# Performance work log

Hardware: AMD Instinct MI355X
Metric: run time of the kernel (lower is better)

Reference implementation:

```python
import jax, jax.numpy as jnp
import numpy as np
import math

B, T, C, NH = 4, 2048, 1024, 16
D = C // NH  # 64, rotary_dim == D

def _rope_tables():
    inv_freq = 1.0 / (10000.0 ** (np.arange(0, D, 2, dtype=np.float32) / D))
    t = np.arange(T, dtype=np.float32)
    freqs = np.outer(t, inv_freq)                 # [T, D/2]
    emb = np.concatenate([freqs, freqs], axis=-1)  # [T, D]
    return jnp.asarray(np.cos(emb))[None], jnp.asarray(np.sin(emb))[None]  # [1,T,D]

def setup_inputs() -> dict:
    key = jax.random.key(0)
    ks = jax.random.split(key, 3)
    x = jax.random.normal(ks[0], (B, T, C), dtype=jnp.float32)
    w_attn = jax.random.normal(ks[1], (3 * C, C), dtype=jnp.float32) * (1.0 / math.sqrt(C))
    b_attn = jnp.zeros((3 * C,), dtype=jnp.float32)
    w_proj = jax.random.normal(ks[2], (C, C), dtype=jnp.float32) * (1.0 / math.sqrt(C))
    b_proj = jnp.zeros((C,), dtype=jnp.float32)
    cos, sin = _rope_tables()
    return {"x": x, "w_attn": w_attn, "b_attn": b_attn,
            "w_proj": w_proj, "b_proj": b_proj, "cos": cos, "sin": sin}

def _rotate_half(u):
    u1, u2 = jnp.split(u, 2, axis=-1)
    return jnp.concatenate([-u2, u1], axis=-1)

def reference(x, w_attn, b_attn, w_proj, b_proj, cos, sin):
    Bx, Tx, Cx = x.shape
    nh, d = NH, Cx // NH
    # fused QKV projection (torch Linear: y = x @ W^T + b)
    qkv = x @ w_attn.T + b_attn                      # [B,T,3C]
    q, k, v = jnp.split(qkv, 3, axis=-1)
    q = q.reshape(Bx, Tx, nh, d).transpose(0, 2, 1, 3)  # [B,nh,T,d]
    k = k.reshape(Bx, Tx, nh, d).transpose(0, 2, 1, 3)
    v = v.reshape(Bx, Tx, nh, d).transpose(0, 2, 1, 3)
    # RoPE (rotary_dim == d, full head)
    c = cos[:, None, :, :]  # [1,1,T,d]
    s = sin[:, None, :, :]
    q = q * c + _rotate_half(q) * s
    k = k * c + _rotate_half(k) * s
    # naive causal attention
    scores = jnp.einsum("bhqd,bhkd->bhqk", q, k) / math.sqrt(d)
    causal = jnp.tril(jnp.ones((Tx, Tx), dtype=bool))
    scores = jnp.where(causal[None, None], scores, -jnp.inf)
    att = jax.nn.softmax(scores, axis=-1)
    y = jnp.einsum("bhqk,bhkd->bhqd", att, v)        # [B,nh,T,d]
    y = y.transpose(0, 2, 1, 3).reshape(Bx, Tx, Cx)
    return y @ w_proj.T + b_proj
```

## Files before the change

kernel.cpp:

```cpp
#include <hip/hip_runtime.h>

typedef __bf16 bf16_t;
typedef bf16_t bf16x8 __attribute__((ext_vector_type(8)));
typedef bf16_t bf16x4 __attribute__((ext_vector_type(4)));
typedef float f32x4 __attribute__((ext_vector_type(4)));

constexpr int BATCH = 4, SEQ = 2048, CH = 1024, NHEAD = 16, HD = 64;
constexpr int BM = 128, BN = 128, BKK = 32;

#define LGKM_FENCE() __asm__ __volatile__("s_waitcnt lgkmcnt(0)" ::: "memory")
#define VM_FENCE() __asm__ __volatile__("s_waitcnt vmcnt(0)" ::: "memory")
#define REORDER_FENCE() __asm__ __volatile__("" ::: "memory")

__device__ __forceinline__ void g2lds16(const bf16_t* g, bf16_t* l) {
  __builtin_amdgcn_global_load_lds((__attribute__((address_space(1))) void*)(g),
                                   (__attribute__((address_space(3))) void*)(l),
                                   16, 0, 0);
}

__device__ __forceinline__ f32x4 mfma16(bf16x8 a, bf16x8 b, f32x4 c) {
  return __builtin_amdgcn_mfma_f32_16x16x32_bf16(a, b, c, 0, 0, 0);
}

__global__ __launch_bounds__(256) void cvt_kernel(const float4* __restrict__ src,
                                                  ushort4* __restrict__ dst, int n4) {
  int i = blockIdx.x * 256 + threadIdx.x;
  if (i >= n4) return;
  float4 f = src[i];
  ushort4 o;
  o.x = __builtin_bit_cast(unsigned short, (bf16_t)f.x);
  o.y = __builtin_bit_cast(unsigned short, (bf16_t)f.y);
  o.z = __builtin_bit_cast(unsigned short, (bf16_t)f.z);
  o.w = __builtin_bit_cast(unsigned short, (bf16_t)f.w);
  dst[i] = o;
}

__device__ __forceinline__ void gemm_mainloop(const bf16_t* __restrict__ A,
                                              const bf16_t* __restrict__ W, int Kdim,
                                              int m0, int n0,
                                              bf16_t* As, bf16_t* Bs,
                                              f32x4 acc[4][4]) {
  const int tid = threadIdx.x;
  const int lane = tid & 63, w = tid >> 6;
  const int quad = lane >> 4, l16 = lane & 15;
  const int wm = (w >> 1) << 6, wn = (w & 1) << 6;
  const int srow = (w << 5) + (lane >> 2);
  const int scol = (lane & 3) << 3;
  const bf16_t* ga0 = A + (size_t)(m0 + srow) * Kdim + scol;
  const bf16_t* ga1 = A + (size_t)(m0 + srow + 16) * Kdim + scol;
  const bf16_t* gb0 = W + (size_t)(n0 + srow) * Kdim + scol;
  const bf16_t* gb1 = W + (size_t)(n0 + srow + 16) * Kdim + scol;
  bf16_t* la0 = As + srow * BKK + scol;
  bf16_t* la1 = As + (srow + 16) * BKK + scol;
  bf16_t* lb0 = Bs + srow * BKK + scol;
  bf16_t* lb1 = Bs + (srow + 16) * BKK + scol;
  for (int k0 = 0; k0 < Kdim; k0 += BKK) {
    g2lds16(ga0 + k0, la0);
    g2lds16(ga1 + k0, la1);
    g2lds16(gb0 + k0, lb0);
    g2lds16(gb1 + k0, lb1);
    VM_FENCE();
    __syncthreads();
    bf16x8 av[4], bv[4];
#pragma unroll
    for (int i = 0; i < 4; i++)
      av[i] = *(const bf16x8*)&As[(wm + i * 16 + l16) * BKK + quad * 8];
#pragma unroll
    for (int i = 0; i < 4; i++)
      bv[i] = *(const bf16x8*)&Bs[(wn + i * 16 + l16) * BKK + quad * 8];
#pragma unroll
    for (int mi = 0; mi < 4; mi++)
#pragma unroll
      for (int ni = 0; ni < 4; ni++)
        acc[mi][ni] = mfma16(av[mi], bv[ni], acc[mi][ni]);
    __syncthreads();
  }
}

constexpr float SCL = 0.125f * 1.44269504089f;

__global__ __launch_bounds__(256) void qkv_rope_kernel(
    const bf16_t* __restrict__ X, const bf16_t* __restrict__ Wa,
    const float* __restrict__ ba, const float* __restrict__ cosT,
    const float* __restrict__ sinT, bf16_t* __restrict__ Q,
    bf16_t* __restrict__ Ko, bf16_t* __restrict__ VT) {
  constexpr int TSTRIDE = 68;
  __shared__ __align__(16) char smem[4 * 64 * TSTRIDE * 2];
  bf16_t* As = (bf16_t*)smem;
  bf16_t* Bs = As + BM * BKK;

  f32x4 acc[4][4];
#pragma unroll
  for (int i = 0; i < 4; i++)
#pragma unroll
    for (int j = 0; j < 4; j++) acc[i][j] = (f32x4){0.f, 0.f, 0.f, 0.f};

  const int n0 = blockIdx.x * BN, m0 = blockIdx.y * BM;
  gemm_mainloop(X, Wa, CH, m0, n0, As, Bs, acc);

  const int tid = threadIdx.x, lane = tid & 63, w = tid >> 6;
  const int quad = lane >> 4, l16 = lane & 15;
  const int wm = (w >> 1) << 6, wn = (w & 1) << 6;
  const int nbase = n0 + wn;
  const int part = nbase >> 10;
  const int h = (nbase & 1023) >> 6;
  const int mbase = m0 + wm;
  const int bb = mbase >> 11;
  const size_t headbase = ((size_t)(bb * NHEAD + h)) * SEQ * HD;

  if (part < 2) {
    bf16_t* O = (part == 0) ? Q : Ko;
    const float post = (part == 0) ? SCL : 1.0f;
#pragma unroll
    for (int mi = 0; mi < 4; mi++)
#pragma unroll
      for (int r = 0; r < 4; r++) {
        int m = mbase + mi * 16 + quad * 4 + r;
        int t = m & (SEQ - 1);
        const float* cr = cosT + t * HD;
        const float* sr = sinT + t * HD;
        size_t rowo = headbase + (size_t)t * HD;
#pragma unroll
        for (int ni = 0; ni < 2; ni++) {
          int d0 = ni * 16 + l16, d1 = d0 + 32;
          float v0 = acc[mi][ni][r] + ba[nbase + d0];
          float v1 = acc[mi][ni + 2][r] + ba[nbase + d1];
          float r0 = (v0 * cr[d0] - v1 * sr[d0]) * post;
          float r1 = (v1 * cr[d1] + v0 * sr[d1]) * post;
          O[rowo + d0] = (bf16_t)r0;
          O[rowo + d1] = (bf16_t)r1;
        }
      }
  } else {
    bf16_t* tb = (bf16_t*)smem + w * 64 * TSTRIDE;
    int t0 = mbase & (SEQ - 1);
#pragma unroll
    for (int mi = 0; mi < 4; mi++)
#pragma unroll
      for (int ni = 0; ni < 4; ni++) {
        int d = ni * 16 + l16;
        float bias = ba[nbase + d];
#pragma unroll
        for (int r = 0; r < 4; r++) {
          float v = acc[mi][ni][r] + bias;
          tb[d * TSTRIDE + mi * 16 + quad * 4 + r] = (bf16_t)v;
        }
      }
    LGKM_FENCE();
    int half = lane >> 5, l5 = lane & 31;
    size_t vbase = ((size_t)(bb * NHEAD + h)) * HD * SEQ;
#pragma unroll
    for (int it = 0; it < 32; it++) {
      int d = it * 2 + half;
      unsigned int val = *(const unsigned int*)&tb[d * TSTRIDE + l5 * 2];
      *(unsigned int*)&VT[vbase + (size_t)d * SEQ + t0 + l5 * 2] = val;
    }
  }
}

__device__ __forceinline__ void sm_update(f32x4 (&s)[4], float& lr,
                                          bf16_t* Prow, int quad,
                                          int swz, bool domask, int lim) {
  if (domask) {
#pragma unroll
    for (int ni = 0; ni < 4; ni++)
#pragma unroll
      for (int r = 0; r < 4; r++)
        if (ni * 16 + r > lim) s[ni][r] = -1e30f;
  }
  float sum = 0.f;
#pragma unroll
  for (int ni = 0; ni < 4; ni++) {
    float p0 = __builtin_exp2f(s[ni][0]);
    float p1 = __builtin_exp2f(s[ni][1]);
    float p2 = __builtin_exp2f(s[ni][2]);
    float p3 = __builtin_exp2f(s[ni][3]);
    bf16x4 pk = {(bf16_t)p0, (bf16_t)p1, (bf16_t)p2, (bf16_t)p3};
    *(bf16x4*)&Prow[(((ni << 2) | quad) ^ (swz << 1)) << 2] = pk;
    sum += (p0 + p1) + (p2 + p3);
  }
  lr += sum;
}

__global__ __launch_bounds__(256) void flash_kernel(const bf16_t* __restrict__ Q,
                                                    const bf16_t* __restrict__ Kg,
                                                    const bf16_t* __restrict__ VT,
                                                    bf16_t* __restrict__ att) {
  __shared__ __align__(16) bf16_t Ks[2][64 * 64];
  __shared__ __align__(16) bf16_t Vs[2][64 * 64];
  __shared__ __align__(16) bf16_t Pt[4][16 * 64];
  const int tid = threadIdx.x, w = tid >> 6, lane = tid & 63;
  const int quad = lane >> 4, l16 = lane & 15;
  const int p = (int)blockIdx.x >> 6;
  const int bh = (int)blockIdx.x & 63;
  const bf16_t* Qp = Q + (size_t)bh * SEQ * HD;
  const bf16_t* Kb = Kg + (size_t)bh * SEQ * HD;
  const bf16_t* Vb = VT + (size_t)bh * HD * SEQ;
  const int grow = lane >> 3;
  const int gj8 = ((lane & 7) ^ grow) * 8;
  const int i0 = w * 2;
  const int sw = l16 & 7;
  const int swz = l16 >> 1;
  const int bloc = bh >> 4, hh = bh & 15;
  bf16_t* Pw = &Pt[w][l16 * 64];
  const int rs0 = (quad ^ swz) << 3;
  const int rs1 = ((4 + quad) ^ swz) << 3;

  auto stage = [&](int kcs, int b) {
#pragma unroll
    for (int ii = 0; ii < 2; ii++) {
      int i = i0 + ii;
      g2lds16(Kb + (size_t)(kcs + i * 8 + grow) * HD + gj8, &Ks[b][(i * 64 + lane) * 8]);
      g2lds16(Vb + (size_t)(i * 8 + grow) * SEQ + kcs + gj8, &Vs[b][(i * 64 + lane) * 8]);
    }
  };

  for (int sp = 0; sp < 2; ++sp) {
    const int j = sp ? p : 31 - p;
    const int m = j * 64 + w * 16;
    const int nch = j + 1;
    bf16x8 aq0 = *(const bf16x8*)&Qp[(size_t)(m + l16) * HD + quad * 8];
    bf16x8 aq1 = *(const bf16x8*)&Qp[(size_t)(m + l16) * HD + 32 + quad * 8];
    float lr = 0.f;
    f32x4 y[4];
#pragma unroll
    for (int ni = 0; ni < 4; ni++) y[ni] = (f32x4){0.f, 0.f, 0.f, 0.f};

    stage(0, 0);
    VM_FENCE();
    __syncthreads();

    for (int c = 0; c < nch; ++c) {
      const int kc = c * 64, buf = c & 1;
      if (c + 1 < nch) stage(kc + 64, buf ^ 1);
      f32x4 s[4];
#pragma unroll
      for (int ni = 0; ni < 4; ni++) {
        bf16x8 k0 = *(const bf16x8*)&Ks[buf][((ni * 16 + l16) * 8 + (quad ^ sw)) * 8];
        bf16x8 k1 = *(const bf16x8*)&Ks[buf][((ni * 16 + l16) * 8 + ((4 + quad) ^ sw)) * 8];
        f32x4 z = (f32x4){0.f, 0.f, 0.f, 0.f};
        s[ni] = mfma16(k1, aq1, mfma16(k0, aq0, z));
      }
      sm_update(s, lr, Pw, quad, swz, c == nch - 1, m + l16 - kc - quad * 4);
      LGKM_FENCE();
      bf16x8 p0 = *(const bf16x8*)&Pw[rs0];
      bf16x8 p1 = *(const bf16x8*)&Pw[rs1];
#pragma unroll
      for (int ni = 0; ni < 4; ni++) {
        bf16x8 v0 = *(const bf16x8*)&Vs[buf][((ni * 16 + l16) * 8 + (quad ^ sw)) * 8];
        bf16x8 v1 = *(const bf16x8*)&Vs[buf][((ni * 16 + l16) * 8 + ((4 + quad) ^ sw)) * 8];
        y[ni] = mfma16(v1, p1, mfma16(v0, p0, y[ni]));
      }
      VM_FENCE();
      __syncthreads();
    }

    lr += __shfl_xor(lr, 16);
    lr += __shfl_xor(lr, 32);
    float inv = 1.f / lr;
    size_t rb = ((size_t)bloc * SEQ + m + l16) * CH + hh * HD + quad * 4;
#pragma unroll
    for (int ni = 0; ni < 4; ni++) {
      bf16x4 o = {(bf16_t)(y[ni][0] * inv), (bf16_t)(y[ni][1] * inv),
                  (bf16_t)(y[ni][2] * inv), (bf16_t)(y[ni][3] * inv)};
      *(bf16x4*)&att[rb + ni * 16] = o;
    }
  }
}

__global__ __launch_bounds__(256) void proj_kernel(const bf16_t* __restrict__ A,
                                                   const bf16_t* __restrict__ Wp,
                                                   const float* __restrict__ bp,
                                                   float* __restrict__ out) {
  __shared__ __align__(16) bf16_t As[BM * BKK];
  __shared__ __align__(16) bf16_t Bs[BN * BKK];
  f32x4 acc[4][4];
#pragma unroll
  for (int i = 0; i < 4; i++)
#pragma unroll
    for (int j = 0; j < 4; j++) acc[i][j] = (f32x4){0.f, 0.f, 0.f, 0.f};
  const int n0 = blockIdx.x * BN, m0 = blockIdx.y * BM;
  gemm_mainloop(A, Wp, CH, m0, n0, As, Bs, acc);
  const int tid = threadIdx.x, lane = tid & 63, w = tid >> 6;
  const int quad = lane >> 4, l16 = lane & 15;
  const int wm = (w >> 1) << 6, wn = (w & 1) << 6;
  const int nbase = n0 + wn, mbase = m0 + wm;
#pragma unroll
  for (int mi = 0; mi < 4; mi++)
#pragma unroll
    for (int r = 0; r < 4; r++) {
      int m = mbase + mi * 16 + quad * 4 + r;
#pragma unroll
      for (int ni = 0; ni < 4; ni++) {
        int n = nbase + ni * 16 + l16;
        out[(size_t)m * CH + n] = acc[mi][ni][r] + bp[n];
      }
    }
}

extern "C" void kernel_launch(void* const* d_in, const int* in_sizes, int n_in,
                              void* d_out, int out_size, void* d_ws, size_t ws_size,
                              hipStream_t stream) {
  const float* x      = (const float*)d_in[0];
  const float* w_attn = (const float*)d_in[1];
  const float* b_attn = (const float*)d_in[2];
  const float* w_proj = (const float*)d_in[3];
  const float* b_proj = (const float*)d_in[4];
  const float* cosT   = (const float*)d_in[5];
  const float* sinT   = (const float*)d_in[6];
  float* out = (float*)d_out;

  bf16_t* xbf  = (bf16_t*)d_ws;
  bf16_t* wabf = xbf + (size_t)8192 * 1024;
  bf16_t* wpbf = wabf + (size_t)3072 * 1024;
  bf16_t* Qb   = wpbf + (size_t)1024 * 1024;
  bf16_t* Kb   = Qb + (size_t)8388608;
  bf16_t* VTb  = Kb + (size_t)8388608;
  bf16_t* attb = VTb + (size_t)8388608;

  cvt_kernel<<<8192, 256, 0, stream>>>((const float4*)x, (ushort4*)xbf, 2097152);
  cvt_kernel<<<3072, 256, 0, stream>>>((const float4*)w_attn, (ushort4*)wabf, 786432);
  cvt_kernel<<<1024, 256, 0, stream>>>((const float4*)w_proj, (ushort4*)wpbf, 262144);
  qkv_rope_kernel<<<dim3(24, 64), 256, 0, stream>>>(xbf, wabf, b_attn, cosT, sinT,
                                                    Qb, Kb, VTb);
  flash_kernel<<<dim3(1024), 256, 0, stream>>>(Qb, Kb, VTb, attb);
  proj_kernel<<<dim3(8, 64), 256, 0, stream>>>(attb, wpbf, b_proj, out);
}
```

Before: 279.8 us.

## Double GEMM K-tile, swizzle LDS, remap blocks across XCDs, fuse conversions

Raises the GEMM K-step to 64 with an XOR-swizzled LDS layout, halving barrier count per K and avoiding bank conflicts on fragment reads. Linearizes the GEMM grids and permutes block ids so consecutive blocks are spread across the 8 XCDs for better L2 locality. Merges the three fp32-to-bf16 conversion launches into one. Uses more LDS per block, which may lower occupancy.

```diff
diff --git a/kernel.cpp b/kernel.cpp
--- a/kernel.cpp
+++ b/kernel.cpp
@@ -6,11 +6,10 @@
 typedef float f32x4 __attribute__((ext_vector_type(4)));
 
 constexpr int BATCH = 4, SEQ = 2048, CH = 1024, NHEAD = 16, HD = 64;
-constexpr int BM = 128, BN = 128, BKK = 32;
+constexpr int BM = 128, BN = 128, BKK = 64;
 
 #define LGKM_FENCE() __asm__ __volatile__("s_waitcnt lgkmcnt(0)" ::: "memory")
 #define VM_FENCE() __asm__ __volatile__("s_waitcnt vmcnt(0)" ::: "memory")
-#define REORDER_FENCE() __asm__ __volatile__("" ::: "memory")
 
 __device__ __forceinline__ void g2lds16(const bf16_t* g, bf16_t* l) {
   __builtin_amdgcn_global_load_lds((__attribute__((address_space(1))) void*)(g),
@@ -22,17 +21,30 @@
   return __builtin_amdgcn_mfma_f32_16x16x32_bf16(a, b, c, 0, 0, 0);
 }
 
-__global__ __launch_bounds__(256) void cvt_kernel(const float4* __restrict__ src,
-                                                  ushort4* __restrict__ dst, int n4) {
-  int i = blockIdx.x * 256 + threadIdx.x;
-  if (i >= n4) return;
-  float4 f = src[i];
+__global__ __launch_bounds__(256) void cvt3_kernel(const float4* __restrict__ x,
+                                                   ushort4* __restrict__ dx,
+                                                   const float4* __restrict__ wa,
+                                                   ushort4* __restrict__ dwa,
+                                                   const float4* __restrict__ wp,
+                                                   ushort4* __restrict__ dwp) {
+  int bid = blockIdx.x;
+  const float4* s;
+  ushort4* d;
+  int i;
+  if (bid < 8192) {
+    s = x; d = dx; i = bid * 256 + threadIdx.x;
+  } else if (bid < 11264) {
+    s = wa; d = dwa; i = (bid - 8192) * 256 + threadIdx.x;
+  } else {
+    s = wp; d = dwp; i = (bid - 11264) * 256 + threadIdx.x;
+  }
+  float4 f = s[i];
   ushort4 o;
   o.x = __builtin_bit_cast(unsigned short, (bf16_t)f.x);
   o.y = __builtin_bit_cast(unsigned short, (bf16_t)f.y);
   o.z = __builtin_bit_cast(unsigned short, (bf16_t)f.z);
   o.w = __builtin_bit_cast(unsigned short, (bf16_t)f.w);
-  dst[i] = o;
+  d[i] = o;
 }
 
 __device__ __forceinline__ void gemm_mainloop(const bf16_t* __restrict__ A,
@@ -41,38 +53,49 @@
                                               bf16_t* As, bf16_t* Bs,
                                               f32x4 acc[4][4]) {
   const int tid = threadIdx.x;
-  const int lane = tid & 63, w = tid >> 6;
+  const int lane = tid & 63;
+  const int w = tid >> 6;
   const int quad = lane >> 4, l16 = lane & 15;
   const int wm = (w >> 1) << 6, wn = (w & 1) << 6;
-  const int srow = (w << 5) + (lane >> 2);
-  const int scol = (lane & 3) << 3;
-  const bf16_t* ga0 = A + (size_t)(m0 + srow) * Kdim + scol;
-  const bf16_t* ga1 = A + (size_t)(m0 + srow + 16) * Kdim + scol;
-  const bf16_t* gb0 = W + (size_t)(n0 + srow) * Kdim + scol;
-  const bf16_t* gb1 = W + (size_t)(n0 + srow + 16) * Kdim + scol;
-  bf16_t* la0 = As + srow * BKK + scol;
-  bf16_t* la1 = As + (srow + 16) * BKK + scol;
-  bf16_t* lb0 = Bs + srow * BKK + scol;
-  bf16_t* lb1 = Bs + (srow + 16) * BKK + scol;
+  const int srow = tid >> 3;
+  const int scol = ((tid & 7) ^ (srow & 7)) << 3;
+  const int dcol = (tid & 7) << 3;
+  const int key = l16 & 15 & 7;
+  const bf16_t* ga[4];
+  const bf16_t* gb[4];
+  bf16_t *la[4], *lb[4];
+#pragma unroll
+  for (int p = 0; p < 4; p++) {
+    int row = p * 32 + srow;
+    ga[p] = A + (size_t)(m0 + row) * Kdim + scol;
+    gb[p] = W + (size_t)(n0 + row) * Kdim + scol;
+    la[p] = As + row * BKK + dcol;
+    lb[p] = Bs + row * BKK + dcol;
+  }
   for (int k0 = 0; k0 < Kdim; k0 += BKK) {
-    g2lds16(ga0 + k0, la0);
-    g2lds16(ga1 + k0, la1);
-    g2lds16(gb0 + k0, lb0);
-    g2lds16(gb1 + k0, lb1);
+#pragma unroll
+    for (int p = 0; p < 4; p++) g2lds16(ga[p] + k0, la[p]);
+#pragma unroll
+    for (int p = 0; p < 4; p++) g2lds16(gb[p] + k0, lb[p]);
     VM_FENCE();
     __syncthreads();
-    bf16x8 av[4], bv[4];
-#pragma unroll
-    for (int i = 0; i < 4; i++)
-      av[i] = *(const bf16x8*)&As[(wm + i * 16 + l16) * BKK + quad * 8];
-#pragma unroll
-    for (int i = 0; i < 4; i++)
-      bv[i] = *(const bf16x8*)&Bs[(wn + i * 16 + l16) * BKK + quad * 8];
-#pragma unroll
-    for (int mi = 0; mi < 4; mi++)
-#pragma unroll
-      for (int ni = 0; ni < 4; ni++)
-        acc[mi][ni] = mfma16(av[mi], bv[ni], acc[mi][ni]);
+#pragma unroll
+    for (int ki = 0; ki < 2; ki++) {
+      bf16x8 av[4], bv[4];
+#pragma unroll
+      for (int i = 0; i < 4; i++)
+        av[i] = *(const bf16x8*)&As[(wm + i * 16 + l16) * BKK +
+                                    ((((ki << 2) | quad) ^ key) << 3)];
+#pragma unroll
+      for (int i = 0; i < 4; i++)
+        bv[i] = *(const bf16x8*)&Bs[(wn + i * 16 + l16) * BKK +
+                                    ((((ki << 2) | quad) ^ key) << 3)];
+#pragma unroll
+      for (int mi = 0; mi < 4; mi++)
+#pragma unroll
+        for (int ni = 0; ni < 4; ni++)
+          acc[mi][ni] = mfma16(av[mi], bv[ni], acc[mi][ni]);
+    }
     __syncthreads();
   }
 }
@@ -95,7 +118,10 @@
 #pragma unroll
     for (int j = 0; j < 4; j++) acc[i][j] = (f32x4){0.f, 0.f, 0.f, 0.f};
 
-  const int n0 = blockIdx.x * BN, m0 = blockIdx.y * BM;
+  const int id = blockIdx.x;
+  const int sid = ((id & 7) * 192) + (id >> 3);
+  const int n0 = (sid % 24) * BN;
+  const int m0 = (sid / 24) * BM;
   gemm_mainloop(X, Wa, CH, m0, n0, As, Bs, acc);
 
   const int tid = threadIdx.x, lane = tid & 63, w = tid >> 6;
@@ -279,7 +305,10 @@
   for (int i = 0; i < 4; i++)
 #pragma unroll
     for (int j = 0; j < 4; j++) acc[i][j] = (f32x4){0.f, 0.f, 0.f, 0.f};
-  const int n0 = blockIdx.x * BN, m0 = blockIdx.y * BM;
+  const int id = blockIdx.x;
+  const int sid = ((id & 7) * 64) + (id >> 3);
+  const int n0 = (sid % 8) * BN;
+  const int m0 = (sid / 8) * BM;
   gemm_mainloop(A, Wp, CH, m0, n0, As, Bs, acc);
   const int tid = threadIdx.x, lane = tid & 63, w = tid >> 6;
   const int quad = lane >> 4, l16 = lane & 15;
@@ -318,11 +347,11 @@
   bf16_t* VTb  = Kb + (size_t)8388608;
   bf16_t* attb = VTb + (size_t)8388608;
 
-  cvt_kernel<<<8192, 256, 0, stream>>>((const float4*)x, (ushort4*)xbf, 2097152);
-  cvt_kernel<<<3072, 256, 0, stream>>>((const float4*)w_attn, (ushort4*)wabf, 786432);
-  cvt_kernel<<<1024, 256, 0, stream>>>((const float4*)w_proj, (ushort4*)wpbf, 262144);
-  qkv_rope_kernel<<<dim3(24, 64), 256, 0, stream>>>(xbf, wabf, b_attn, cosT, sinT,
-                                                    Qb, Kb, VTb);
+  cvt3_kernel<<<12288, 256, 0, stream>>>((const float4*)x, (ushort4*)xbf,
+                                         (const float4*)w_attn, (ushort4*)wabf,
+                                         (const float4*)w_proj, (ushort4*)wpbf);
+  qkv_rope_kernel<<<dim3(1536), 256, 0, stream>>>(xbf, wabf, b_attn, cosT, sinT,
+                                                  Qb, Kb, VTb);
   flash_kernel<<<dim3(1024), 256, 0, stream>>>(Qb, Kb, VTb, attb);
-  proj_kernel<<<dim3(8, 64), 256, 0, stream>>>(attb, wpbf, b_proj, out);
-}
+  proj_kernel<<<dim3(512), 256, 0, stream>>>(attb, wpbf, b_proj, out);
+}
```

New measurement: 266.8 us. 1.05x faster.
